# Kernel optimization log

Hardware: AMD Instinct MI355X
Metric: run time of the kernel (lower is better)

Reference implementation:

```python
import jax, jax.numpy as jnp
import numpy as np
from jax import lax

B_COEF = 0.25  # commitment loss weight
NUM_EMB = 1024
EMB_DIM = 64


def setup_inputs() -> dict:
    key = jax.random.key(0)
    k1, k2 = jax.random.split(key)
    z_e = jax.random.normal(k1, (32, EMB_DIM, 64, 64), dtype=jnp.float32)
    # codebook init: uniform(-1/num_emb, 1/num_emb) as in torch module
    emb = jax.random.uniform(k2, (NUM_EMB, EMB_DIM), dtype=jnp.float32,
                             minval=-1.0 / NUM_EMB, maxval=1.0 / NUM_EMB)
    return {"z_e": z_e, "emb": emb}


def reference(z_e, emb):
    b, c, h, w = z_e.shape  # c == emb_dim
    # (b,c,h,w) -> (b*h*w, c)
    z_flat = jnp.transpose(z_e, (0, 2, 3, 1)).reshape(b * h * w, c)
    # squared euclidean distance: ||z||^2 + ||e||^2 - 2 z.e^T
    dist = (jnp.sum(z_flat ** 2, axis=-1, keepdims=True)
            + jnp.sum(emb ** 2, axis=-1)[None, :]
            - 2.0 * jnp.matmul(z_flat, emb.T))
    enc_idx = jnp.argmin(dist, axis=-1)  # [b*h*w]
    z_q = emb[enc_idx].reshape(b, h, w, c)  # gather
    z_q = jnp.transpose(z_q, (0, 3, 1, 2))  # (b,c,h,w)
    reconstruction_loss = jnp.mean((z_q - lax.stop_gradient(z_e)) ** 2)
    commitment_loss = B_COEF * jnp.mean((lax.stop_gradient(z_q) - z_e) ** 2)
    loss = reconstruction_loss + commitment_loss
    # straight-through estimator
    z_q_st = z_e + lax.stop_gradient(z_q - z_e)
    return z_q_st, loss, enc_idx
```

## Files before the change

### kernel.cpp

```cpp
#include <hip/hip_runtime.h>
#include <hip/hip_bf16.h>

#define NUM_EMB 1024
#define EMB_DIM 64
#define NPIX    131072
#define ZQ_ELEMS 8388608
#define KDEPTH  16
#define ZSTRIDE 65
#define NACC    64
#define BIAS    0.25f


typedef __attribute__((ext_vector_type(8))) short short8_t;
typedef __attribute__((ext_vector_type(4))) float f32x4;

__device__ __forceinline__ unsigned umin32(unsigned a, unsigned b) { return a < b ? a : b; }
__device__ __forceinline__ unsigned umax32(unsigned a, unsigned b) { return a > b ? a : b; }

__device__ __forceinline__ float np_sumsq64(const float* __restrict__ x) {
    float q[EMB_DIM];
    #pragma unroll
    for (int c = 0; c < EMB_DIM; ++c) q[c] = x[c] * x[c];
    float r0 = q[0], r1 = q[1], r2 = q[2], r3 = q[3];
    float r4 = q[4], r5 = q[5], r6 = q[6], r7 = q[7];
    #pragma unroll
    for (int g = 1; g < 8; ++g) {
        r0 += q[8 * g + 0]; r1 += q[8 * g + 1];
        r2 += q[8 * g + 2]; r3 += q[8 * g + 3];
        r4 += q[8 * g + 4]; r5 += q[8 * g + 5];
        r6 += q[8 * g + 6]; r7 += q[8 * g + 7];
    }
    return ((r0 + r1) + (r2 + r3)) + ((r4 + r5) + (r6 + r7));
}

__device__ __forceinline__ unsigned long long packvk(float v, int k) {
    unsigned u = __float_as_uint(v);
    u = (u & 0x80000000u) ? ~u : (u | 0x80000000u);
    return ((unsigned long long)u << 32) | (unsigned)k;
}

__device__ __forceinline__ float np_score(const float* __restrict__ emb, int k,
                                          const float* __restrict__ zl,
                                          float zzv, float e2k) {
    const float4* ek4 = (const float4*)(emb + k * EMB_DIM);
    float acc = 0.f;
    #pragma unroll
    for (int c4 = 0; c4 < 16; ++c4) {
        float4 e4 = ek4[c4];
        acc = fmaf(e4.x, zl[c4 * 4 + 0], acc);
        acc = fmaf(e4.y, zl[c4 * 4 + 1], acc);
        acc = fmaf(e4.z, zl[c4 * 4 + 2], acc);
        acc = fmaf(e4.w, zl[c4 * 4 + 3], acc);
    }
    return (zzv + e2k) - 2.0f * acc;
}

__global__ __launch_bounds__(256) void vq_prep(const float* __restrict__ emb,
                                               short* __restrict__ wsE,
                                               float* __restrict__ wsE2,
                                               float* __restrict__ wsAcc) {
    #pragma clang fp contract(off)
    int t    = blockIdx.x * 256 + threadIdx.x;
    if (blockIdx.x == 0 && threadIdx.x < NACC) wsAcc[threadIdx.x] = 0.f;
    int l    = t & 63;
    int ch   = (t >> 6) & 15;
    int q    = t >> 10;
    int code = q * 256 + ch * 16 + (l & 15);
    const float* ek = emb + code * EMB_DIM;
    #pragma unroll
    for (int h = 0; h < 2; ++h) {
        short8_t pk;
        #pragma unroll
        for (int j = 0; j < 8; ++j) {
            int chan = 32 * h + 8 * (l >> 4) + j;
            __hip_bfloat16 bv = __float2bfloat16(-2.0f * ek[chan]);
            unsigned short u; __builtin_memcpy(&u, &bv, 2);
            pk[j] = (short)u;
        }
        *(short8_t*)(wsE + t * 16 + h * 8) = pk;
    }
    if (t < NUM_EMB) wsE2[t] = np_sumsq64(emb + t * EMB_DIM);
}

__global__ __launch_bounds__(256, 4) void vq_mfma(const float* __restrict__ z_e,
                                                  const float* __restrict__ emb,
                                                  const short* __restrict__ wsE,
                                                  const float* __restrict__ wsE2,
                                                  float* __restrict__ zq_out,
                                                  float* __restrict__ enc_out,
                                                  float* __restrict__ wsAcc) {
    #pragma clang fp contract(off)
    __shared__ float sZf[64 * ZSTRIDE];
    __shared__ float sE2[NUM_EMB];
    __shared__ unsigned sMinP[4][64];
    __shared__ float sBand[64];
    __shared__ float sThrF[64];
    __shared__ unsigned sThrP[64];
    __shared__ float sZZ[64];
    __shared__ unsigned long long sBestPack[64];
    __shared__ unsigned short sKbuf[64][KDEPTH];
    __shared__ int   sKcnt[64];
    __shared__ int   sPxFlag[64];
    __shared__ int   sFlagAny;

    const int tid  = threadIdx.x;
    const int w    = tid >> 6;
    const int lane = tid & 63;
    const int p0   = blockIdx.x * 64;
    const int b    = p0 >> 12;
    const int hw0  = p0 & 4095;
    const float* base = z_e + (size_t)b * (EMB_DIM * 4096) + hw0;

    *(f32x4*)&sE2[tid * 4] = *(const f32x4*)&wsE2[tid * 4];
    if (tid < 64) { sKcnt[tid] = 0; sBestPack[tid] = ~0ULL; sPxFlag[tid] = 0; }
    if (tid == 0) sFlagAny = 0;

    {
        const float* zp = base + lane;
        float v[16];
        #pragma unroll
        for (int j = 0; j < 16; ++j) v[j] = zp[(size_t)(16 * w + j) * 4096];
        #pragma unroll
        for (int j = 0; j < 16; ++j) sZf[lane * ZSTRIDE + 16 * w + j] = v[j];
    }
    __syncthreads();

    if (w == 0) {
        const float* zl = &sZf[lane * ZSTRIDE];
        float rr[8] = {0,0,0,0,0,0,0,0};
        float sab = 0.f;
        #pragma unroll
        for (int g = 0; g < 8; ++g)
            #pragma unroll
            for (int j = 0; j < 8; ++j) {
                float zc = zl[8 * g + j];
                float qq = zc * zc;
                rr[j] += qq;
                sab += fabsf(zc);
            }
        sZZ[lane]   = ((rr[0] + rr[1]) + (rr[2] + rr[3])) + ((rr[4] + rr[5]) + (rr[6] + rr[7]));
        sBand[lane] = 2.0f * (9e-6f * sab + 2e-5f) + 1e-4f;
    }

    short8_t bfrag[4][2];
    #pragma unroll
    for (int pg = 0; pg < 4; ++pg)
        #pragma unroll
        for (int h = 0; h < 2; ++h) {
            int bpr = pg * 16 + (lane & 15);
            int c0  = 32 * h + 8 * (lane >> 4);
            short8_t pk;
            #pragma unroll
            for (int j = 0; j < 8; ++j) {
                __hip_bfloat16 bv = __float2bfloat16(sZf[bpr * ZSTRIDE + c0 + j]);
                unsigned short u; __builtin_memcpy(&u, &bv, 2);
                pk[j] = (short)u;
            }
            asm volatile("" : "+v"(pk));
            bfrag[pg][h] = pk;
        }

    const short8_t* ef = (const short8_t*)wsE + (size_t)w * 2048;

    unsigned p1[4] = {~0u, ~0u, ~0u, ~0u};
    unsigned p2[4] = {~0u, ~0u, ~0u, ~0u};
    unsigned p3[4] = {~0u, ~0u, ~0u, ~0u};
    {
        short8_t A0a = ef[(0 * 64 + lane) * 2 + 0];
        short8_t A1a = ef[(0 * 64 + lane) * 2 + 1];
        short8_t A0b = ef[(1 * 64 + lane) * 2 + 0];
        short8_t A1b = ef[(1 * 64 + lane) * 2 + 1];
        #pragma unroll 1
        for (int ch = 0; ch < 16; ch += 2) {
            {
                int chn = ch + 2 < 16 ? ch + 2 : 15;
                short8_t N0 = ef[(chn * 64 + lane) * 2 + 0];
                short8_t N1 = ef[(chn * 64 + lane) * 2 + 1];
                int kbase = w * 256 + ch * 16 + 4 * (lane >> 4);
                f32x4 e2v = *(const f32x4*)(&sE2[kbase]);
                f32x4 e2bv;
                e2bv[0] = e2v[0] + BIAS; e2bv[1] = e2v[1] + BIAS;
                e2bv[2] = e2v[2] + BIAS; e2bv[3] = e2v[3] + BIAS;
                unsigned kb[4] = {(unsigned)kbase, (unsigned)kbase + 1u,
                                  (unsigned)kbase + 2u, (unsigned)kbase + 3u};
                #pragma unroll
                for (int pg = 0; pg < 4; ++pg) {
                    f32x4 acc = __builtin_amdgcn_mfma_f32_16x16x32_bf16(A0a, bfrag[pg][0], e2bv, 0, 0, 0);
                    acc = __builtin_amdgcn_mfma_f32_16x16x32_bf16(A1a, bfrag[pg][1], acc, 0, 0, 0);
                    #pragma unroll
                    for (int j = 0; j < 4; ++j) {
                        unsigned t  = (__float_as_uint(acc[j]) & 0xFFFFFC00u) | kb[j];
                        unsigned n1 = umin32(p1[pg], t);
                        unsigned x1 = umax32(p1[pg], t);
                        unsigned n2 = umin32(p2[pg], x1);
                        unsigned x2 = umax32(p2[pg], x1);
                        unsigned n3 = umin32(p3[pg], x2);
                        p1[pg] = n1; p2[pg] = n2; p3[pg] = n3;
                    }
                }
                A0a = N0; A1a = N1;
            }
            {
                int chn = ch + 3 < 16 ? ch + 3 : 15;
                short8_t N0 = ef[(chn * 64 + lane) * 2 + 0];
                short8_t N1 = ef[(chn * 64 + lane) * 2 + 1];
                int kbase = w * 256 + (ch + 1) * 16 + 4 * (lane >> 4);
                f32x4 e2v = *(const f32x4*)(&sE2[kbase]);
                f32x4 e2bv;
                e2bv[0] = e2v[0] + BIAS; e2bv[1] = e2v[1] + BIAS;
                e2bv[2] = e2v[2] + BIAS; e2bv[3] = e2v[3] + BIAS;
                unsigned kb[4] = {(unsigned)kbase, (unsigned)kbase + 1u,
                                  (unsigned)kbase + 2u, (unsigned)kbase + 3u};
                #pragma unroll
                for (int pg = 0; pg < 4; ++pg) {
                    f32x4 acc = __builtin_amdgcn_mfma_f32_16x16x32_bf16(A0b, bfrag[pg][0], e2bv, 0, 0, 0);
                    acc = __builtin_amdgcn_mfma_f32_16x16x32_bf16(A1b, bfrag[pg][1], acc, 0, 0, 0);
                    #pragma unroll
                    for (int j = 0; j < 4; ++j) {
                        unsigned t  = (__float_as_uint(acc[j]) & 0xFFFFFC00u) | kb[j];
                        unsigned n1 = umin32(p1[pg], t);
                        unsigned x1 = umax32(p1[pg], t);
                        unsigned n2 = umin32(p2[pg], x1);
                        unsigned x2 = umax32(p2[pg], x1);
                        unsigned n3 = umin32(p3[pg], x2);
                        p1[pg] = n1; p2[pg] = n2; p3[pg] = n3;
                    }
                }
                A0b = N0; A1b = N1;
            }
        }
    }

    #pragma unroll
    for (int pg = 0; pg < 4; ++pg) {
        unsigned g = p1[pg];
        g = umin32(g, (unsigned)__shfl_xor((int)g, 16, 64));
        g = umin32(g, (unsigned)__shfl_xor((int)g, 32, 64));
        if (lane < 16) sMinP[w][pg * 16 + lane] = g;
    }
    __syncthreads();
    if (tid < 64) {
        unsigned gp = umin32(umin32(sMinP[0][tid], sMinP[1][tid]),
                             umin32(sMinP[2][tid], sMinP[3][tid]));
        float m    = __uint_as_float(gp & 0xFFFFFC00u);
        float thrF = m + sBand[tid];
        sThrF[tid] = thrF;
        sThrP[tid] = (__float_as_uint(thrF) & 0xFFFFFC00u) | 1023u;
    }
    __syncthreads();

    #pragma unroll
    for (int pg = 0; pg < 4; ++pg) {
        int px = pg * 16 + (lane & 15);
        unsigned thrp = sThrP[px];
        int n = (p1[pg] <= thrp) + (p2[pg] <= thrp) + (p3[pg] <= thrp);
        if (n) {
            int slot = atomicAdd(&sKcnt[px], n);
            if (slot < KDEPTH)                     sKbuf[px][slot]     = (unsigned short)(p1[pg] & 1023u);
            if (n >= 2 && slot + 1 < KDEPTH)       sKbuf[px][slot + 1] = (unsigned short)(p2[pg] & 1023u);
            if (n >= 3) {
                if (slot + 2 < KDEPTH)             sKbuf[px][slot + 2] = (unsigned short)(p3[pg] & 1023u);
                sPxFlag[px] = 1; sFlagAny = 1;
            }
        }
    }
    __syncthreads();

    if (sFlagAny) {
        if (tid < 64 && sPxFlag[tid]) sKcnt[tid] = 0;
        __syncthreads();
        float thrB[4];
        #pragma unroll
        for (int pg = 0; pg < 4; ++pg) {
            int px = pg * 16 + (lane & 15);
            thrB[pg] = sPxFlag[px] ? sThrF[px] : -1e30f;
        }
        short8_t A0a = ef[(0 * 64 + lane) * 2 + 0];
        short8_t A1a = ef[(0 * 64 + lane) * 2 + 1];
        short8_t A0b = ef[(1 * 64 + lane) * 2 + 0];
        short8_t A1b = ef[(1 * 64 + lane) * 2 + 1];
        #pragma unroll 1
        for (int ch = 0; ch < 16; ch += 2) {
            {
                int chn = ch + 2 < 16 ? ch + 2 : 15;
                short8_t N0 = ef[(chn * 64 + lane) * 2 + 0];
                short8_t N1 = ef[(chn * 64 + lane) * 2 + 1];
                int kbase = w * 256 + ch * 16 + 4 * (lane >> 4);
                f32x4 e2v = *(const f32x4*)(&sE2[kbase]);
                f32x4 e2bv;
                e2bv[0] = e2v[0] + BIAS; e2bv[1] = e2v[1] + BIAS;
                e2bv[2] = e2v[2] + BIAS; e2bv[3] = e2v[3] + BIAS;
                #pragma unroll
                for (int pg = 0; pg < 4; ++pg) {
                    f32x4 acc = __builtin_amdgcn_mfma_f32_16x16x32_bf16(A0a, bfrag[pg][0], e2bv, 0, 0, 0);
                    acc = __builtin_amdgcn_mfma_f32_16x16x32_bf16(A1a, bfrag[pg][1], acc, 0, 0, 0);
                    #pragma unroll
                    for (int j = 0; j < 4; ++j) {
                        if (acc[j] <= thrB[pg]) {
                            int pix  = pg * 16 + (lane & 15);
                            int slot = atomicAdd(&sKcnt[pix], 1);
                            if (slot < KDEPTH) sKbuf[pix][slot] = (unsigned short)(kbase + j);
                        }
                    }
                }
                A0a = N0; A1a = N1;
            }
            {
                int chn = ch + 3 < 16 ? ch + 3 : 15;
                short8_t N0 = ef[(chn * 64 + lane) * 2 + 0];
                short8_t N1 = ef[(chn * 64 + lane) * 2 + 1];
                int kbase = w * 256 + (ch + 1) * 16 + 4 * (lane >> 4);
                f32x4 e2v = *(const f32x4*)(&sE2[kbase]);
                f32x4 e2bv;
                e2bv[0] = e2v[0] + BIAS; e2bv[1] = e2v[1] + BIAS;
                e2bv[2] = e2v[2] + BIAS; e2bv[3] = e2v[3] + BIAS;
                #pragma unroll
                for (int pg = 0; pg < 4; ++pg) {
                    f32x4 acc = __builtin_amdgcn_mfma_f32_16x16x32_bf16(A0b, bfrag[pg][0], e2bv, 0, 0, 0);
                    acc = __builtin_amdgcn_mfma_f32_16x16x32_bf16(A1b, bfrag[pg][1], acc, 0, 0, 0);
                    #pragma unroll
                    for (int j = 0; j < 4; ++j) {
                        if (acc[j] <= thrB[pg]) {
                            int pix  = pg * 16 + (lane & 15);
                            int slot = atomicAdd(&sKcnt[pix], 1);
                            if (slot < KDEPTH) sKbuf[pix][slot] = (unsigned short)(kbase + j);
                        }
                    }
                }
                A0b = N0; A1b = N1;
            }
        }
        __syncthreads();
    }

    {
        const int px = lane;
        const float* zl = &sZf[px * ZSTRIDE];
        float zzv = sZZ[px];
        int rawcnt = sKcnt[px];
        if (rawcnt == 1) {
            if (w == 0) sBestPack[px] = packvk(-1e30f, (int)sKbuf[px][0]);
        } else if (rawcnt <= KDEPTH) {
            for (int s = w; s < rawcnt; s += 4) {
                int k = (int)sKbuf[px][s];
                float v = np_score(emb, k, zl, zzv, sE2[k]);
                atomicMin(&sBestPack[px], packvk(v, k));
            }
        } else {
            for (int k = w; k < NUM_EMB; k += 4) {
                float v = np_score(emb, k, zl, zzv, sE2[k]);
                atomicMin(&sBestPack[px], packvk(v, k));
            }
        }
    }
    __syncthreads();

    if (tid < 64)
        enc_out[p0 + tid] = (float)(unsigned)(sBestPack[tid] & 0xFFFFFFFFull);
    {
        const int px = lane;
        int bestk = (int)(sBestPack[px] & 0xFFFFFFFFull);
        const float4* eq4 = (const float4*)(emb + bestk * EMB_DIM) + 4 * w;
        const float* zl = &sZf[px * ZSTRIDE];
        float* op = zq_out + (size_t)b * (EMB_DIM * 4096) + hw0 + px;
        float ls = 0.f;
        #pragma unroll
        for (int j4 = 0; j4 < 4; ++j4) {
            float4 e4 = eq4[j4];
            int c = 16 * w + j4 * 4;
            float d0 = e4.x - zl[c + 0];
            float d1 = e4.y - zl[c + 1];
            float d2 = e4.z - zl[c + 2];
            float d3 = e4.w - zl[c + 3];
            ls = fmaf(d0, d0, ls);
            ls = fmaf(d1, d1, ls);
            ls = fmaf(d2, d2, ls);
            ls = fmaf(d3, d3, ls);
            op[(size_t)(c + 0) * 4096] = e4.x;
            op[(size_t)(c + 1) * 4096] = e4.y;
            op[(size_t)(c + 2) * 4096] = e4.z;
            op[(size_t)(c + 3) * 4096] = e4.w;
        }
        #pragma unroll
        for (int off = 32; off > 0; off >>= 1) ls += __shfl_down(ls, off, 64);
        if (lane == 0) atomicAdd(&wsAcc[blockIdx.x & (NACC - 1)], ls);
    }
}

__global__ void vq_final_ws(const float* __restrict__ wsAcc,
                            float* __restrict__ loss_out) {
    int lane = threadIdx.x;
    float v = wsAcc[lane];
    #pragma unroll
    for (int off = 32; off > 0; off >>= 1) v += __shfl_down(v, off, 64);
    if (lane == 0) loss_out[0] = v * (1.25f / (float)ZQ_ELEMS);
}

__global__ void vq_final_direct(float* __restrict__ loss_out) {
    loss_out[0] = loss_out[0] * (1.25f / (float)ZQ_ELEMS);
}

__global__ __launch_bounds__(256) void vq_nn_fb(const float* __restrict__ z_e,
                                                const float* __restrict__ emb,
                                                float* __restrict__ zq_out,
                                                float* __restrict__ enc_out,
                                                float* __restrict__ loss_acc) {
    #pragma clang fp contract(off)
    __shared__ float s_e2[NUM_EMB];
    int tid = threadIdx.x;
    for (int k = tid; k < NUM_EMB; k += 256) s_e2[k] = np_sumsq64(emb + k * EMB_DIM);
    __syncthreads();
    int p = blockIdx.x * 256 + tid;
    int b = p >> 12, hw = p & 4095;
    const float* zp = z_e + (size_t)b * (EMB_DIM * 4096) + hw;
    float z[EMB_DIM];
    #pragma unroll
    for (int c = 0; c < EMB_DIM; ++c) z[c] = zp[(size_t)c * 4096];
    float zz = np_sumsq64(z);
    float b1 = 3.4e38f; int i1 = 0;
    #pragma unroll 2
    for (int k = 0; k < NUM_EMB; ++k) {
        const float* ek = emb + k * EMB_DIM;
        float acc = 0.f;
        #pragma unroll
        for (int c = 0; c < EMB_DIM; ++c) acc = fmaf(ek[c], z[c], acc);
        float sc = (zz + s_e2[k]) - 2.0f * acc;
        bool lt = sc < b1; b1 = lt ? sc : b1; i1 = lt ? k : i1;
    }
    const float* eq = emb + i1 * EMB_DIM;
    float* op = zq_out + (size_t)b * (EMB_DIM * 4096) + hw;
    float ls = 0.f;
    #pragma unroll
    for (int c = 0; c < EMB_DIM; ++c) {
        float q = eq[c]; float d = q - z[c];
        ls = fmaf(d, d, ls);
        op[(size_t)c * 4096] = q;
    }
    enc_out[p] = (float)i1;
    #pragma unroll
    for (int off = 32; off > 0; off >>= 1) ls += __shfl_down(ls, off, 64);
    if ((tid & 63) == 0) atomicAdd(loss_acc, ls);
}

extern "C" void kernel_launch(void* const* d_in, const int* in_sizes, int n_in,
                              void* d_out, int out_size, void* d_ws, size_t ws_size,
                              hipStream_t stream) {
    const float* z_e = (const float*)d_in[0];
    const float* emb = (const float*)d_in[1];
    float* out = (float*)d_out;
    float* loss_out = out + ZQ_ELEMS;
    float* enc_out  = out + ZQ_ELEMS + 1;

    if (ws_size >= 140 * 1024) {
        short* wsE   = (short*)d_ws;
        float* wsE2  = (float*)((char*)d_ws + 131072);
        float* wsAcc = (float*)((char*)d_ws + 135168);
        vq_prep<<<16, 256, 0, stream>>>(emb, wsE, wsE2, wsAcc);
        vq_mfma<<<NPIX / 64, 256, 0, stream>>>(z_e, emb, wsE, wsE2, out, enc_out, wsAcc);
        vq_final_ws<<<1, 64, 0, stream>>>(wsAcc, loss_out);
    } else {
        hipMemsetAsync(loss_out, 0, 4, stream);
        vq_nn_fb<<<NPIX / 256, 256, 0, stream>>>(z_e, emb, out, enc_out, loss_out);
        vq_final_direct<<<1, 1, 0, stream>>>(loss_out);
    }
}
```

Before: 85.98 us.

## Process 128 pixels per block to reuse codebook fragments across more pixel groups

Doubles the per-block pixel tile from 64 to 128 (8 MFMA pixel groups per wave), so each codebook fragment loaded from global memory feeds twice as many MFMAs and the grid halves. The per-pixel refinement and output phases are remapped onto two halves of the block, and the rescan loop is simplified to a single-buffered prefetch. Launch bounds drop to 3 blocks per CU to make room for the larger register footprint (doubled bfrag and top-3 state), which lowers occupancy and may reduce latency hiding.

```diff
diff --git a/kernel.cpp b/kernel.cpp
--- a/kernel.cpp
+++ b/kernel.cpp
@@ -9,6 +9,8 @@
 #define ZSTRIDE 65
 #define NACC    64
 #define BIAS    0.25f
+#define PXB     128
+#define NPG     8
 
 
 typedef __attribute__((ext_vector_type(8))) short short8_t;
@@ -82,7 +84,7 @@
     if (t < NUM_EMB) wsE2[t] = np_sumsq64(emb + t * EMB_DIM);
 }
 
-__global__ __launch_bounds__(256, 4) void vq_mfma(const float* __restrict__ z_e,
+__global__ __launch_bounds__(256, 3) void vq_mfma(const float* __restrict__ z_e,
                                                   const float* __restrict__ emb,
                                                   const short* __restrict__ wsE,
                                                   const float* __restrict__ wsE2,
@@ -90,43 +92,45 @@
                                                   float* __restrict__ enc_out,
                                                   float* __restrict__ wsAcc) {
     #pragma clang fp contract(off)
-    __shared__ float sZf[64 * ZSTRIDE];
+    __shared__ float sZf[PXB * ZSTRIDE];
     __shared__ float sE2[NUM_EMB];
-    __shared__ unsigned sMinP[4][64];
-    __shared__ float sBand[64];
-    __shared__ float sThrF[64];
-    __shared__ unsigned sThrP[64];
-    __shared__ float sZZ[64];
-    __shared__ unsigned long long sBestPack[64];
-    __shared__ unsigned short sKbuf[64][KDEPTH];
-    __shared__ int   sKcnt[64];
-    __shared__ int   sPxFlag[64];
+    __shared__ unsigned sMinP[4][PXB];
+    __shared__ float sBand[PXB];
+    __shared__ float sThrF[PXB];
+    __shared__ unsigned sThrP[PXB];
+    __shared__ float sZZ[PXB];
+    __shared__ unsigned long long sBestPack[PXB];
+    __shared__ unsigned short sKbuf[PXB][KDEPTH];
+    __shared__ int   sKcnt[PXB];
+    __shared__ int   sPxFlag[PXB];
     __shared__ int   sFlagAny;
 
     const int tid  = threadIdx.x;
     const int w    = tid >> 6;
     const int lane = tid & 63;
-    const int p0   = blockIdx.x * 64;
+    const int p0   = blockIdx.x * PXB;
     const int b    = p0 >> 12;
     const int hw0  = p0 & 4095;
     const float* base = z_e + (size_t)b * (EMB_DIM * 4096) + hw0;
 
     *(f32x4*)&sE2[tid * 4] = *(const f32x4*)&wsE2[tid * 4];
-    if (tid < 64) { sKcnt[tid] = 0; sBestPack[tid] = ~0ULL; sPxFlag[tid] = 0; }
+    if (tid < PXB) { sKcnt[tid] = 0; sBestPack[tid] = ~0ULL; sPxFlag[tid] = 0; }
     if (tid == 0) sFlagAny = 0;
 
     {
-        const float* zp = base + lane;
-        float v[16];
-        #pragma unroll
-        for (int j = 0; j < 16; ++j) v[j] = zp[(size_t)(16 * w + j) * 4096];
-        #pragma unroll
-        for (int j = 0; j < 16; ++j) sZf[lane * ZSTRIDE + 16 * w + j] = v[j];
-    }
-    __syncthreads();
-
-    if (w == 0) {
-        const float* zl = &sZf[lane * ZSTRIDE];
+        const int px = tid & (PXB - 1);
+        const int cg = tid >> 7;
+        const float* zp = base + px;
+        float v[32];
+        #pragma unroll
+        for (int j = 0; j < 32; ++j) v[j] = zp[(size_t)(32 * cg + j) * 4096];
+        #pragma unroll
+        for (int j = 0; j < 32; ++j) sZf[px * ZSTRIDE + 32 * cg + j] = v[j];
+    }
+    __syncthreads();
+
+    if (tid < PXB) {
+        const float* zl = &sZf[tid * ZSTRIDE];
         float rr[8] = {0,0,0,0,0,0,0,0};
         float sab = 0.f;
         #pragma unroll
@@ -138,13 +142,13 @@
                 rr[j] += qq;
                 sab += fabsf(zc);
             }
-        sZZ[lane]   = ((rr[0] + rr[1]) + (rr[2] + rr[3])) + ((rr[4] + rr[5]) + (rr[6] + rr[7]));
-        sBand[lane] = 2.0f * (9e-6f * sab + 2e-5f) + 1e-4f;
-    }
-
-    short8_t bfrag[4][2];
-    #pragma unroll
-    for (int pg = 0; pg < 4; ++pg)
+        sZZ[tid]   = ((rr[0] + rr[1]) + (rr[2] + rr[3])) + ((rr[4] + rr[5]) + (rr[6] + rr[7]));
+        sBand[tid] = 2.0f * (9e-6f * sab + 2e-5f) + 1e-4f;
+    }
+
+    short8_t bfrag[NPG][2];
+    #pragma unroll
+    for (int pg = 0; pg < NPG; ++pg)
         #pragma unroll
         for (int h = 0; h < 2; ++h) {
             int bpr = pg * 16 + (lane & 15);
@@ -162,9 +166,9 @@
 
     const short8_t* ef = (const short8_t*)wsE + (size_t)w * 2048;
 
-    unsigned p1[4] = {~0u, ~0u, ~0u, ~0u};
-    unsigned p2[4] = {~0u, ~0u, ~0u, ~0u};
-    unsigned p3[4] = {~0u, ~0u, ~0u, ~0u};
+    unsigned p1[NPG], p2[NPG], p3[NPG];
+    #pragma unroll
+    for (int pg = 0; pg < NPG; ++pg) { p1[pg] = ~0u; p2[pg] = ~0u; p3[pg] = ~0u; }
     {
         short8_t A0a = ef[(0 * 64 + lane) * 2 + 0];
         short8_t A1a = ef[(0 * 64 + lane) * 2 + 1];
@@ -184,7 +188,7 @@
                 unsigned kb[4] = {(unsigned)kbase, (unsigned)kbase + 1u,
                                   (unsigned)kbase + 2u, (unsigned)kbase + 3u};
                 #pragma unroll
-                for (int pg = 0; pg < 4; ++pg) {
+                for (int pg = 0; pg < NPG; ++pg) {
                     f32x4 acc = __builtin_amdgcn_mfma_f32_16x16x32_bf16(A0a, bfrag[pg][0], e2bv, 0, 0, 0);
                     acc = __builtin_amdgcn_mfma_f32_16x16x32_bf16(A1a, bfrag[pg][1], acc, 0, 0, 0);
                     #pragma unroll
@@ -212,7 +216,7 @@
                 unsigned kb[4] = {(unsigned)kbase, (unsigned)kbase + 1u,
                                   (unsigned)kbase + 2u, (unsigned)kbase + 3u};
                 #pragma unroll
-                for (int pg = 0; pg < 4; ++pg) {
+                for (int pg = 0; pg < NPG; ++pg) {
                     f32x4 acc = __builtin_amdgcn_mfma_f32_16x16x32_bf16(A0b, bfrag[pg][0], e2bv, 0, 0, 0);
                     acc = __builtin_amdgcn_mfma_f32_16x16x32_bf16(A1b, bfrag[pg][1], acc, 0, 0, 0);
                     #pragma unroll
@@ -232,14 +236,14 @@
     }
 
     #pragma unroll
-    for (int pg = 0; pg < 4; ++pg) {
+    for (int pg = 0; pg < NPG; ++pg) {
         unsigned g = p1[pg];
         g = umin32(g, (unsigned)__shfl_xor((int)g, 16, 64));
         g = umin32(g, (unsigned)__shfl_xor((int)g, 32, 64));
         if (lane < 16) sMinP[w][pg * 16 + lane] = g;
     }
     __syncthreads();
-    if (tid < 64) {
+    if (tid < PXB) {
         unsigned gp = umin32(umin32(sMinP[0][tid], sMinP[1][tid]),
                              umin32(sMinP[2][tid], sMinP[3][tid]));
         float m    = __uint_as_float(gp & 0xFFFFFC00u);
@@ -250,7 +254,7 @@
     __syncthreads();
 
     #pragma unroll
-    for (int pg = 0; pg < 4; ++pg) {
+    for (int pg = 0; pg < NPG; ++pg) {
         int px = pg * 16 + (lane & 15);
         unsigned thrp = sThrP[px];
         int n = (p1[pg] <= thrp) + (p2[pg] <= thrp) + (p3[pg] <= thrp);
@@ -267,87 +271,60 @@
     __syncthreads();
 
     if (sFlagAny) {
-        if (tid < 64 && sPxFlag[tid]) sKcnt[tid] = 0;
+        if (tid < PXB && sPxFlag[tid]) sKcnt[tid] = 0;
         __syncthreads();
-        float thrB[4];
-        #pragma unroll
-        for (int pg = 0; pg < 4; ++pg) {
+        float thrB[NPG];
+        #pragma unroll
+        for (int pg = 0; pg < NPG; ++pg) {
             int px = pg * 16 + (lane & 15);
             thrB[pg] = sPxFlag[px] ? sThrF[px] : -1e30f;
         }
-        short8_t A0a = ef[(0 * 64 + lane) * 2 + 0];
-        short8_t A1a = ef[(0 * 64 + lane) * 2 + 1];
-        short8_t A0b = ef[(1 * 64 + lane) * 2 + 0];
-        short8_t A1b = ef[(1 * 64 + lane) * 2 + 1];
+        short8_t A0 = ef[lane * 2 + 0];
+        short8_t A1 = ef[lane * 2 + 1];
         #pragma unroll 1
-        for (int ch = 0; ch < 16; ch += 2) {
-            {
-                int chn = ch + 2 < 16 ? ch + 2 : 15;
-                short8_t N0 = ef[(chn * 64 + lane) * 2 + 0];
-                short8_t N1 = ef[(chn * 64 + lane) * 2 + 1];
-                int kbase = w * 256 + ch * 16 + 4 * (lane >> 4);
-                f32x4 e2v = *(const f32x4*)(&sE2[kbase]);
-                f32x4 e2bv;
-                e2bv[0] = e2v[0] + BIAS; e2bv[1] = e2v[1] + BIAS;
-                e2bv[2] = e2v[2] + BIAS; e2bv[3] = e2v[3] + BIAS;
+        for (int ch = 0; ch < 16; ++ch) {
+            int chn = ch < 15 ? ch + 1 : 15;
+            short8_t N0 = ef[(chn * 64 + lane) * 2 + 0];
+            short8_t N1 = ef[(chn * 64 + lane) * 2 + 1];
+            int kbase = w * 256 + ch * 16 + 4 * (lane >> 4);
+            f32x4 e2v = *(const f32x4*)(&sE2[kbase]);
+            f32x4 e2bv;
+            e2bv[0] = e2v[0] + BIAS; e2bv[1] = e2v[1] + BIAS;
+            e2bv[2] = e2v[2] + BIAS; e2bv[3] = e2v[3] + BIAS;
+            #pragma unroll
+            for (int pg = 0; pg < NPG; ++pg) {
+                f32x4 acc = __builtin_amdgcn_mfma_f32_16x16x32_bf16(A0, bfrag[pg][0], e2bv, 0, 0, 0);
+                acc = __builtin_amdgcn_mfma_f32_16x16x32_bf16(A1, bfrag[pg][1], acc, 0, 0, 0);
                 #pragma unroll
-                for (int pg = 0; pg < 4; ++pg) {
-                    f32x4 acc = __builtin_amdgcn_mfma_f32_16x16x32_bf16(A0a, bfrag[pg][0], e2bv, 0, 0, 0);
-                    acc = __builtin_amdgcn_mfma_f32_16x16x32_bf16(A1a, bfrag[pg][1], acc, 0, 0, 0);
-                    #pragma unroll
-                    for (int j = 0; j < 4; ++j) {
-                        if (acc[j] <= thrB[pg]) {
-                            int pix  = pg * 16 + (lane & 15);
-                            int slot = atomicAdd(&sKcnt[pix], 1);
-                            if (slot < KDEPTH) sKbuf[pix][slot] = (unsigned short)(kbase + j);
-                        }
+                for (int j = 0; j < 4; ++j) {
+                    if (acc[j] <= thrB[pg]) {
+                        int pix  = pg * 16 + (lane & 15);
+                        int slot = atomicAdd(&sKcnt[pix], 1);
+                        if (slot < KDEPTH) sKbuf[pix][slot] = (unsigned short)(kbase + j);
                     }
                 }
-                A0a = N0; A1a = N1;
-            }
-            {
-                int chn = ch + 3 < 16 ? ch + 3 : 15;
-                short8_t N0 = ef[(chn * 64 + lane) * 2 + 0];
-                short8_t N1 = ef[(chn * 64 + lane) * 2 + 1];
-                int kbase = w * 256 + (ch + 1) * 16 + 4 * (lane >> 4);
-                f32x4 e2v = *(const f32x4*)(&sE2[kbase]);
-                f32x4 e2bv;
-                e2bv[0] = e2v[0] + BIAS; e2bv[1] = e2v[1] + BIAS;
-                e2bv[2] = e2v[2] + BIAS; e2bv[3] = e2v[3] + BIAS;
-                #pragma unroll
-                for (int pg = 0; pg < 4; ++pg) {
-                    f32x4 acc = __builtin_amdgcn_mfma_f32_16x16x32_bf16(A0b, bfrag[pg][0], e2bv, 0, 0, 0);
-                    acc = __builtin_amdgcn_mfma_f32_16x16x32_bf16(A1b, bfrag[pg][1], acc, 0, 0, 0);
-                    #pragma unroll
-                    for (int j = 0; j < 4; ++j) {
-                        if (acc[j] <= thrB[pg]) {
-                            int pix  = pg * 16 + (lane & 15);
-                            int slot = atomicAdd(&sKcnt[pix], 1);
-                            if (slot < KDEPTH) sKbuf[pix][slot] = (unsigned short)(kbase + j);
-                        }
-                    }
-                }
-                A0b = N0; A1b = N1;
-            }
+            }
+            A0 = N0; A1 = N1;
         }
         __syncthreads();
     }
 
     {
-        const int px = lane;
+        const int px   = tid & (PXB - 1);
+        const int half = tid >> 7;
         const float* zl = &sZf[px * ZSTRIDE];
         float zzv = sZZ[px];
         int rawcnt = sKcnt[px];
         if (rawcnt == 1) {
-            if (w == 0) sBestPack[px] = packvk(-1e30f, (int)sKbuf[px][0]);
+            if (half == 0) sBestPack[px] = packvk(-1e30f, (int)sKbuf[px][0]);
         } else if (rawcnt <= KDEPTH) {
-            for (int s = w; s < rawcnt; s += 4) {
+            for (int s = half; s < rawcnt; s += 2) {
                 int k = (int)sKbuf[px][s];
                 float v = np_score(emb, k, zl, zzv, sE2[k]);
                 atomicMin(&sBestPack[px], packvk(v, k));
             }
         } else {
-            for (int k = w; k < NUM_EMB; k += 4) {
+            for (int k = half; k < NUM_EMB; k += 2) {
                 float v = np_score(emb, k, zl, zzv, sE2[k]);
                 atomicMin(&sBestPack[px], packvk(v, k));
             }
@@ -355,19 +332,20 @@
     }
     __syncthreads();
 
-    if (tid < 64)
+    if (tid < PXB)
         enc_out[p0 + tid] = (float)(unsigned)(sBestPack[tid] & 0xFFFFFFFFull);
     {
-        const int px = lane;
+        const int px   = tid & (PXB - 1);
+        const int cg   = tid >> 7;
         int bestk = (int)(sBestPack[px] & 0xFFFFFFFFull);
-        const float4* eq4 = (const float4*)(emb + bestk * EMB_DIM) + 4 * w;
+        const float4* eq4 = (const float4*)(emb + bestk * EMB_DIM) + 8 * cg;
         const float* zl = &sZf[px * ZSTRIDE];
         float* op = zq_out + (size_t)b * (EMB_DIM * 4096) + hw0 + px;
         float ls = 0.f;
         #pragma unroll
-        for (int j4 = 0; j4 < 4; ++j4) {
+        for (int j4 = 0; j4 < 8; ++j4) {
             float4 e4 = eq4[j4];
-            int c = 16 * w + j4 * 4;
+            int c = 32 * cg + j4 * 4;
             float d0 = e4.x - zl[c + 0];
             float d1 = e4.y - zl[c + 1];
             float d2 = e4.z - zl[c + 2];
@@ -456,7 +434,7 @@
         float* wsE2  = (float*)((char*)d_ws + 131072);
         float* wsAcc = (float*)((char*)d_ws + 135168);
         vq_prep<<<16, 256, 0, stream>>>(emb, wsE, wsE2, wsAcc);
-        vq_mfma<<<NPIX / 64, 256, 0, stream>>>(z_e, emb, wsE, wsE2, out, enc_out, wsAcc);
+        vq_mfma<<<NPIX / PXB, 256, 0, stream>>>(z_e, emb, wsE, wsE2, out, enc_out, wsAcc);
         vq_final_ws<<<1, 64, 0, stream>>>(wsAcc, loss_out);
     } else {
         hipMemsetAsync(loss_out, 0, 4, stream);
```

Result: faster. 79.94 us (-7.0%).
